# Optimization experiments

Hardware: AMD Instinct MI355X
Metric: run time of the kernel (lower is better)

## Reference

```python
import jax, jax.numpy as jnp
import numpy as np

N = 100000      # nodes
E = 1600000     # edges
NINP = 64       # input node features
NE = 8          # edge attr channels (spectral supports)
NOUT = 24       # nout1 == nout2
NIN = 2 * NOUT  # 48, hidden width after concat
G = 256         # graphs in batch
EPS = 1e-5


def setup_inputs() -> dict:
    key = jax.random.key(0)
    ks = jax.random.split(key, 40)
    def nrm(i, shape, s=1.0):
        return jax.random.normal(ks[i], shape, dtype=jnp.float32) * s
    inp = {}
    inp["x"] = nrm(0, (N, NINP))
    inp["edge_index"] = jax.random.randint(ks[1], (2, E), 0, N)
    inp["edge_attr"] = nrm(2, (E, NE))
    inp["batch"] = jnp.sort(jax.random.randint(ks[3], (N,), 0, G))
    i = 4
    for l, din in ((1, NINP), (2, NIN), (3, NIN)):
        inp[f"W{l}"] = nrm(i, (NE, din, NOUT), 0.1); i += 1   # SpectConv weight [K,in,out]
        inp[f"b{l}"] = jnp.zeros((NOUT,), jnp.float32)         # SpectConv bias
        inp[f"A{l}"] = nrm(i, (din, NOUT), 0.1); i += 1        # fc11 weight
        inp[f"a{l}"] = jnp.zeros((NOUT,), jnp.float32)
        inp[f"B{l}"] = nrm(i, (din, NOUT), 0.1); i += 1        # fc12 weight
        inp[f"c{l}"] = jnp.zeros((NOUT,), jnp.float32)
        inp[f"g{l}"] = jnp.ones((NIN,), jnp.float32)           # BN gamma
        inp[f"be{l}"] = jnp.zeros((NIN,), jnp.float32)         # BN beta
    inp["F1"] = nrm(i, (NIN, 32), 0.1); i += 1
    inp["f1"] = jnp.zeros((32,), jnp.float32)
    inp["F2"] = nrm(i, (32, 1), 0.1); i += 1
    inp["f2"] = jnp.zeros((1,), jnp.float32)
    return inp


def _ml3(x, src, dst, ea, W, b, A, a, Bm, c):
    # SpectConv (selfconn=False): sum_k segment_sum(ea[:,k]*x[src] -> dst) @ W[k] + b
    xs = x[src]                                    # [E, F] gather
    acc = jnp.zeros((x.shape[0], W.shape[2]), x.dtype)
    for k in range(W.shape[0]):                    # small fixed K=NE loop
        h = jax.ops.segment_sum(ea[:, k:k+1] * xs, dst, num_segments=x.shape[0])
        acc = acc + h @ W[k]
    conv = jax.nn.relu(acc + b)
    gate = jax.nn.relu(x @ A + a) * jnp.tanh(x @ Bm + c)
    return jnp.concatenate([conv, gate], axis=1)   # [N, NIN]


def _bn(x, g, b):
    # BatchNorm1d, training mode (biased batch statistics)
    m = x.mean(0)
    v = x.var(0)
    return (x - m) * jax.lax.rsqrt(v + EPS) * g + b


def reference(x, edge_index, edge_attr, batch,
              W1, b1, A1, a1, B1, c1, g1, be1,
              W2, b2, A2, a2, B2, c2, g2, be2,
              W3, b3, A3, a3, B3, c3, g3, be3,
              F1, f1, F2, f2):
    src, dst = edge_index[0], edge_index[1]
    h = _bn(_ml3(x, src, dst, edge_attr, W1, b1, A1, a1, B1, c1), g1, be1)
    h = _bn(_ml3(h, src, dst, edge_attr, W2, b2, A2, a2, B2, c2), g2, be2)
    h = _bn(_ml3(h, src, dst, edge_attr, W3, b3, A3, a3, B3, c3), g3, be3)
    sums = jax.ops.segment_sum(h, batch, num_segments=G)
    cnts = jax.ops.segment_sum(jnp.ones((h.shape[0], 1), h.dtype), batch, num_segments=G)
    pooled = sums / jnp.maximum(cnts, 1.0)         # global_mean_pool
    return jax.nn.relu(pooled @ F1 + f1) @ F2 + f2  # [G, 1]
```

## Files before the change

kernel.cpp:

```cpp
#include <hip/hip_runtime.h>
#include <hip/hip_fp16.h>
#include <math.h>

#define N_NODES 100000
#define N_EDGES 1600000
#define NGRAPH  256
#define YCOLS   240
#define EPS     1e-5f
#define BNCHUNK 200

typedef _Float16 h2v  __attribute__((ext_vector_type(2)));
typedef _Float16 f16x8 __attribute__((ext_vector_type(8)));
typedef float    f32x4 __attribute__((ext_vector_type(4)));

#if defined(__has_builtin)
#if __has_builtin(__builtin_amdgcn_fdot2)
#define HAVE_FDOT2 1
#endif
#endif

__device__ inline float dot8(float4 yraw, float4 eraw, float acc) {
#ifdef HAVE_FDOT2
  union U { float4 f; h2v v[4]; } y, e;
  y.f = yraw; e.f = eraw;
  acc = __builtin_amdgcn_fdot2(y.v[0], e.v[0], acc, false);
  acc = __builtin_amdgcn_fdot2(y.v[1], e.v[1], acc, false);
  acc = __builtin_amdgcn_fdot2(y.v[2], e.v[2], acc, false);
  acc = __builtin_amdgcn_fdot2(y.v[3], e.v[3], acc, false);
#else
  const __half2* yh = reinterpret_cast<const __half2*>(&yraw);
  const __half2* eh = reinterpret_cast<const __half2*>(&eraw);
#pragma unroll
  for (int i = 0; i < 4; i++) {
    float2 a = __half22float2(yh[i]), b = __half22float2(eh[i]);
    acc += a.x * b.x + a.y * b.y;
  }
#endif
  return acc;
}

__global__ void k_count(const int* __restrict__ dst, int* __restrict__ deg) {
  int e = blockIdx.x * blockDim.x + threadIdx.x;
  if (e < N_EDGES) atomicAdd(&deg[dst[e]], 1);
}

__global__ void k_scan1(const int* __restrict__ deg, int* __restrict__ part,
                        int* __restrict__ bsum) {
  __shared__ int lds[256];
  int t = threadIdx.x;
  int base = blockIdx.x * 1024 + t * 4;
  int v[4]; int s = 0;
#pragma unroll
  for (int i = 0; i < 4; i++) { int idx = base + i; v[i] = (idx < N_NODES) ? deg[idx] : 0; s += v[i]; }
  lds[t] = s; __syncthreads();
  for (int off = 1; off < 256; off <<= 1) {
    int x = (t >= off) ? lds[t - off] : 0;
    __syncthreads();
    lds[t] += x;
    __syncthreads();
  }
  int excl = lds[t] - s;
#pragma unroll
  for (int i = 0; i < 4; i++) { int idx = base + i; if (idx < N_NODES) part[idx] = excl; excl += v[i]; }
  if (t == 255) bsum[blockIdx.x] = lds[255];
}

__global__ void k_scan2(int* __restrict__ bsum, int nb) {
  __shared__ int lds[128];
  int t = threadIdx.x;
  int v = (t < nb) ? bsum[t] : 0;
  lds[t] = v; __syncthreads();
  for (int off = 1; off < 128; off <<= 1) {
    int x = (t >= off) ? lds[t - off] : 0;
    __syncthreads();
    lds[t] += x;
    __syncthreads();
  }
  if (t < nb) bsum[t] = lds[t] - v;
}

__global__ void k_scan3(int* __restrict__ rowptr, const int* __restrict__ bsum,
                        int* __restrict__ cursor) {
  int i = blockIdx.x * blockDim.x + threadIdx.x;
  if (i < N_NODES) {
    int v = rowptr[i] + bsum[i >> 10];
    rowptr[i] = v; cursor[i] = v;
  }
  if (i == 0) rowptr[N_NODES] = N_EDGES;
}

__global__ void k_fill(const int* __restrict__ src, const int* __restrict__ dst,
                       const float* __restrict__ ea, int* __restrict__ cursor,
                       int* __restrict__ esrc, __half* __restrict__ ea_csr) {
  int e = blockIdx.x * blockDim.x + threadIdx.x;
  if (e < N_EDGES) {
    int d = dst[e];
    int pos = atomicAdd(&cursor[d], 1);
    esrc[pos] = src[e];
    float4 a = *reinterpret_cast<const float4*>(ea + (size_t)e * 8);
    float4 b = *reinterpret_cast<const float4*>(ea + (size_t)e * 8 + 4);
    union { __half h[8]; float4 f; } u;
    u.h[0] = __float2half(a.x); u.h[1] = __float2half(a.y);
    u.h[2] = __float2half(a.z); u.h[3] = __float2half(a.w);
    u.h[4] = __float2half(b.x); u.h[5] = __float2half(b.y);
    u.h[6] = __float2half(b.z); u.h[7] = __float2half(b.w);
    *reinterpret_cast<float4*>(ea_csr + (size_t)pos * 8) = u.f;
  }
}

__global__ void k_ghist(const int* __restrict__ batch, int* __restrict__ gcnt) {
  __shared__ int lh[NGRAPH];
  int t = threadIdx.x;
  lh[t] = 0; __syncthreads();
  for (int i = blockIdx.x * 256 + t; i < N_NODES; i += gridDim.x * 256)
    atomicAdd(&lh[batch[i]], 1);
  __syncthreads();
  if (lh[t]) atomicAdd(&gcnt[t], lh[t]);
}

__global__ void k_gscan(const int* __restrict__ gcnt, int* __restrict__ gstart) {
  __shared__ int lds[NGRAPH];
  int t = threadIdx.x;
  int v = gcnt[t]; lds[t] = v; __syncthreads();
  for (int off = 1; off < NGRAPH; off <<= 1) {
    int x = (t >= off) ? lds[t - off] : 0;
    __syncthreads();
    lds[t] += x;
    __syncthreads();
  }
  gstart[t] = lds[t] - v;
  if (t == NGRAPH - 1) gstart[NGRAPH] = lds[NGRAPH - 1];
}

__global__ void k_wcat_h(const float* __restrict__ W, const float* __restrict__ A,
                         const float* __restrict__ B, __half* __restrict__ out,
                         int din) {
  int i = blockIdx.x * blockDim.x + threadIdx.x;
  if (i >= YCOLS * 64) return;
  int j = i / 64, f = i % 64;
  float v = 0.f;
  if (f < din) {
    if (j < 192)      { int k8 = j / 24, o = j - k8 * 24; v = W[(k8 * din + f) * 24 + o]; }
    else if (j < 216) v = A[f * 24 + (j - 192)];
    else              v = B[f * 24 + (j - 216)];
  }
  out[i] = __float2half(v);
}

template <int F>
__global__ __launch_bounds__(256) void k_mm(const float* __restrict__ X,
                                            const __half* __restrict__ Wct,
                                            const float* __restrict__ ss,
                                            const float* __restrict__ ba,
                                            const float* __restrict__ bc,
                                            __half* __restrict__ Yh,
                                            float* __restrict__ h) {
  __shared__ _Float16 sx[64][64];
  __shared__ _Float16 sy[64][200];
  __shared__ float    sg[64][52];
  int t = threadIdx.x;
  int r0 = blockIdx.x * 64;
  constexpr int F4 = F / 4;
  for (int i = t; i < 64 * F4; i += 256) {
    int row = i / F4, c4 = i - row * F4;
    int grow = r0 + row;
    float4 v = make_float4(0.f, 0.f, 0.f, 0.f);
    if (grow < N_NODES) {
      v = *reinterpret_cast<const float4*>(X + (size_t)grow * F + c4 * 4);
      if (ss) {
        int f = c4 * 4;
        v.x = v.x * ss[f + 0] + ss[48 + f + 0];
        v.y = v.y * ss[f + 1] + ss[48 + f + 1];
        v.z = v.z * ss[f + 2] + ss[48 + f + 2];
        v.w = v.w * ss[f + 3] + ss[48 + f + 3];
      }
    }
    int c = c4 * 4;
    sx[row][c + 0] = (_Float16)v.x;
    sx[row][c + 1] = (_Float16)v.y;
    sx[row][c + 2] = (_Float16)v.z;
    sx[row][c + 3] = (_Float16)v.w;
  }
  if (F == 48) {
    for (int i = t; i < 64 * 16; i += 256) {
      int row = i / 16, k = 48 + (i % 16);
      sx[row][k] = (_Float16)0.f;
    }
  }
  __syncthreads();

  int w = t >> 6, l = t & 63;
  int lrow = l & 15;
  int lk = (l >> 4) * 8;
  const f16x8 a0 = *reinterpret_cast<const f16x8*>(&sx[w * 16 + lrow][lk]);
  const f16x8 a1 = *reinterpret_cast<const f16x8*>(&sx[w * 16 + lrow][lk + 32]);
  const _Float16* wct = reinterpret_cast<const _Float16*>(Wct);

#pragma unroll
  for (int ct = 0; ct < 15; ct++) {
    int col = ct * 16 + lrow;
    f16x8 b0 = *reinterpret_cast<const f16x8*>(wct + col * 64 + lk);
    f16x8 b1 = *reinterpret_cast<const f16x8*>(wct + col * 64 + lk + 32);
    f32x4 acc = {0.f, 0.f, 0.f, 0.f};
    acc = __builtin_amdgcn_mfma_f32_16x16x32_f16(a0, b0, acc, 0, 0, 0);
    acc = __builtin_amdgcn_mfma_f32_16x16x32_f16(a1, b1, acc, 0, 0, 0);
    int ycol = (col % 24) * 8 + col / 24;
    int gc   = (col < 216) ? (col - 192) : (24 + col - 216);
#pragma unroll
    for (int r = 0; r < 4; r++) {
      int row = w * 16 + (l >> 4) * 4 + r;
      if (col < 192) sy[row][ycol] = (_Float16)acc[r];
      else           sg[row][gc] = acc[r];
    }
  }
  __syncthreads();

  int rows = N_NODES - r0; if (rows > 64) rows = 64;
  for (int i = t; i < rows * 48; i += 256) {
    int row = i / 48, c = (i % 48) * 4;
    *reinterpret_cast<uint2*>(Yh + (size_t)(r0 + row) * 192 + c) =
        *reinterpret_cast<const uint2*>(&sy[row][c]);
  }
  for (int i = t; i < rows * 24; i += 256) {
    int row = i / 24, o = i % 24;
    float gate = fmaxf(sg[row][o] + ba[o], 0.f) * tanhf(sg[row][24 + o] + bc[o]);
    h[(size_t)(r0 + row) * 48 + 24 + o] = gate;
  }
}

__global__ __launch_bounds__(192) void k_agg(
    const __half* __restrict__ Yh, const int* __restrict__ rowptr,
    const int* __restrict__ esrc, const __half* __restrict__ ea_csr,
    const float* __restrict__ bconv, float* __restrict__ h) {
  __shared__ float lacc[2][4][24];
  int t = threadIdx.x;
  int ln   = t / 96;
  int slot = (t / 24) % 4;
  int o    = t % 24;
  int n = blockIdx.x * 2 + ln;
  float acc = 0.f;
  if (n < N_NODES) {
    int r0 = rowptr[n], r1 = rowptr[n + 1];
    int idx = r0 + slot;
    for (; idx + 12 < r1; idx += 16) {
      int s0 = esrc[idx], s1 = esrc[idx + 4], s2 = esrc[idx + 8], s3 = esrc[idx + 12];
      float4 e0 = *reinterpret_cast<const float4*>(ea_csr + (size_t)idx * 8);
      float4 e1 = *reinterpret_cast<const float4*>(ea_csr + (size_t)(idx + 4) * 8);
      float4 e2 = *reinterpret_cast<const float4*>(ea_csr + (size_t)(idx + 8) * 8);
      float4 e3 = *reinterpret_cast<const float4*>(ea_csr + (size_t)(idx + 12) * 8);
      float4 y0 = *reinterpret_cast<const float4*>(Yh + (size_t)s0 * 192 + o * 8);
      float4 y1 = *reinterpret_cast<const float4*>(Yh + (size_t)s1 * 192 + o * 8);
      float4 y2 = *reinterpret_cast<const float4*>(Yh + (size_t)s2 * 192 + o * 8);
      float4 y3 = *reinterpret_cast<const float4*>(Yh + (size_t)s3 * 192 + o * 8);
      acc = dot8(y0, e0, acc);
      acc = dot8(y1, e1, acc);
      acc = dot8(y2, e2, acc);
      acc = dot8(y3, e3, acc);
    }
    for (; idx < r1; idx += 4) {
      int s0 = esrc[idx];
      float4 e0 = *reinterpret_cast<const float4*>(ea_csr + (size_t)idx * 8);
      float4 y0 = *reinterpret_cast<const float4*>(Yh + (size_t)s0 * 192 + o * 8);
      acc = dot8(y0, e0, acc);
    }
  }
  lacc[ln][slot][o] = acc;
  __syncthreads();
  if (t < 48) {
    int ln2 = t / 24, oo = t % 24;
    int n2 = blockIdx.x * 2 + ln2;
    if (n2 < N_NODES) {
      float a = lacc[ln2][0][oo] + lacc[ln2][1][oo] + lacc[ln2][2][oo] + lacc[ln2][3][oo];
      h[(size_t)n2 * 48 + oo] = fmaxf(a + bconv[oo], 0.f);
    }
  }
}

__global__ __launch_bounds__(192) void k_bnred1(const float* __restrict__ h,
                                                float* __restrict__ out) {
  __shared__ float lsum[192], lsq[192];
  int t = threadIdx.x;
  int rp = t / 48, c = t % 48;
  int r0 = blockIdx.x * BNCHUNK;
  int r1 = r0 + BNCHUNK; if (r1 > N_NODES) r1 = N_NODES;
  float s = 0.f, q = 0.f;
  for (int r = r0 + rp; r < r1; r += 4) {
    float v = h[(size_t)r * 48 + c];
    s += v; q += v * v;
  }
  lsum[t] = s; lsq[t] = q; __syncthreads();
  if (t < 48) {
    float S = lsum[t] + lsum[t + 48] + lsum[t + 96] + lsum[t + 144];
    float Q = lsq[t] + lsq[t + 48] + lsq[t + 96] + lsq[t + 144];
    out[(size_t)blockIdx.x * 96 + t] = S;
    out[(size_t)blockIdx.x * 96 + 48 + t] = Q;
  }
}

__global__ void k_bnstats(const float* __restrict__ partial, int nblk,
                          const float* __restrict__ g, const float* __restrict__ be,
                          float* __restrict__ ss) {
  __shared__ float ls[256], lq[256];
  int c = blockIdx.x, t = threadIdx.x;
  float s = 0.f, q = 0.f;
  for (int i = t; i < nblk; i += 256) { s += partial[(size_t)i * 96 + c]; q += partial[(size_t)i * 96 + 48 + c]; }
  ls[t] = s; lq[t] = q; __syncthreads();
  for (int off = 128; off > 0; off >>= 1) {
    if (t < off) { ls[t] += ls[t + off]; lq[t] += lq[t + off]; }
    __syncthreads();
  }
  if (t == 0) {
    float mean = ls[0] / (float)N_NODES;
    float var = lq[0] / (float)N_NODES - mean * mean;
    var = fmaxf(var, 0.f);
    float sc = g[c] * rsqrtf(var + EPS);
    ss[c] = sc;
    ss[48 + c] = be[c] - mean * sc;
  }
}

__global__ __launch_bounds__(240) void k_pool2(const float* __restrict__ h,
                                               const int* __restrict__ gstart,
                                               const float* __restrict__ ss,
                                               float* __restrict__ pooled) {
  __shared__ float acc[240];
  int g = blockIdx.x, t = threadIdx.x;
  int o = t % 48, r = t / 48;
  int n0 = gstart[g], n1 = gstart[g + 1];
  float s = 0.f;
  for (int n = n0 + r; n < n1; n += 5) s += h[(size_t)n * 48 + o];
  acc[t] = s; __syncthreads();
  if (t < 48) {
    float tot = acc[t] + acc[t + 48] + acc[t + 96] + acc[t + 144] + acc[t + 192];
    float cnt = (float)(n1 - n0);
    float mean = tot / fmaxf(cnt, 1.f);
    pooled[g * 48 + t] = mean * ss[t] + ss[48 + t];
  }
}

__global__ __launch_bounds__(64) void k_mlp(const float* __restrict__ pooled,
                                            const float* __restrict__ F1,
                                            const float* __restrict__ f1,
                                            const float* __restrict__ F2,
                                            const float* __restrict__ f2,
                                            float* __restrict__ out) {
  __shared__ float p[48];
  int g = blockIdx.x, t = threadIdx.x;
  if (t < 48) p[t] = pooled[g * 48 + t];
  __syncthreads();
  float r = 0.f;
  if (t < 32) {
    float s = f1[t];
#pragma unroll
    for (int c = 0; c < 48; c++) s += p[c] * F1[c * 32 + t];
    r = fmaxf(s, 0.f) * F2[t];
  }
  for (int off = 32; off > 0; off >>= 1) r += __shfl_down(r, off, 64);
  if (t == 0) out[g] = r + f2[0];
}

extern "C" void kernel_launch(void* const* d_in, const int* in_sizes, int n_in,
                              void* d_out, int out_size, void* d_ws, size_t ws_size,
                              hipStream_t stream) {
  const float* x          = (const float*)d_in[0];
  const int*   edge_index = (const int*)d_in[1];
  const float* ea         = (const float*)d_in[2];
  const int*   batch      = (const int*)d_in[3];
  const float *W[3], *bcv[3], *A[3], *ba[3], *B[3], *bc[3], *g[3], *be[3];
  for (int l = 0; l < 3; l++) {
    int base = 4 + l * 8;
    W[l]   = (const float*)d_in[base + 0];
    bcv[l] = (const float*)d_in[base + 1];
    A[l]   = (const float*)d_in[base + 2];
    ba[l]  = (const float*)d_in[base + 3];
    B[l]   = (const float*)d_in[base + 4];
    bc[l]  = (const float*)d_in[base + 5];
    g[l]   = (const float*)d_in[base + 6];
    be[l]  = (const float*)d_in[base + 7];
  }
  const float* F1 = (const float*)d_in[28];
  const float* f1 = (const float*)d_in[29];
  const float* F2 = (const float*)d_in[30];
  const float* f2 = (const float*)d_in[31];
  const int* src = edge_index;
  const int* dst = edge_index + N_EDGES;

  char* w = (char*)d_ws;
  auto alloc = [&](size_t bytes) -> char* {
    char* p = w;
    w += (bytes + 255) & ~(size_t)255;
    return p;
  };
  int nagg = (N_NODES + 1) / 2;
  int nred = (N_NODES + BNCHUNK - 1) / BNCHUNK;

  int*    rowptr  = (int*)alloc((N_NODES + 1) * 4);
  int*    cursor  = (int*)alloc((size_t)N_NODES * 4);
  int*    deg     = (int*)alloc((size_t)N_NODES * 4);
  int*    bsum    = (int*)alloc(128 * 4);
  int*    esrc    = (int*)alloc((size_t)N_EDGES * 4);
  __half* ea_csr  = (__half*)alloc((size_t)N_EDGES * 8 * 2);
  int*    gcnt    = (int*)alloc(NGRAPH * 4);
  int*    gstart  = (int*)alloc((NGRAPH + 1) * 4);
  __half* Wct1    = (__half*)alloc((size_t)YCOLS * 64 * 2);
  __half* Wct2    = (__half*)alloc((size_t)YCOLS * 64 * 2);
  __half* Wct3    = (__half*)alloc((size_t)YCOLS * 64 * 2);
  __half* Yh      = (__half*)alloc((size_t)N_NODES * 192 * 2);
  float*  h0      = (float*)alloc((size_t)N_NODES * 48 * 4);
  float*  h1      = (float*)alloc((size_t)N_NODES * 48 * 4);
  float*  partial2= (float*)alloc((size_t)nred * 96 * 4);
  float*  ss1     = (float*)alloc(96 * 4);
  float*  ss2     = (float*)alloc(96 * 4);
  float*  ss3     = (float*)alloc(96 * 4);
  float*  pooled  = (float*)alloc(NGRAPH * 48 * 4);

  hipMemsetAsync(deg, 0, (size_t)N_NODES * 4, stream);
  hipMemsetAsync(gcnt, 0, NGRAPH * 4, stream);

  k_count<<<(N_EDGES + 255) / 256, 256, 0, stream>>>(dst, deg);
  int nchunk = (N_NODES + 1023) / 1024;
  k_scan1<<<nchunk, 256, 0, stream>>>(deg, rowptr, bsum);
  k_scan2<<<1, 128, 0, stream>>>(bsum, nchunk);
  k_scan3<<<(N_NODES + 255) / 256, 256, 0, stream>>>(rowptr, bsum, cursor);
  k_fill<<<(N_EDGES + 255) / 256, 256, 0, stream>>>(src, dst, ea, cursor, esrc, ea_csr);

  k_ghist<<<64, 256, 0, stream>>>(batch, gcnt);
  k_gscan<<<1, NGRAPH, 0, stream>>>(gcnt, gstart);

  k_wcat_h<<<(YCOLS * 64 + 255) / 256, 256, 0, stream>>>(W[0], A[0], B[0], Wct1, 64);
  k_wcat_h<<<(YCOLS * 64 + 255) / 256, 256, 0, stream>>>(W[1], A[1], B[1], Wct2, 48);
  k_wcat_h<<<(YCOLS * 64 + 255) / 256, 256, 0, stream>>>(W[2], A[2], B[2], Wct3, 48);

  int nmm = (N_NODES + 63) / 64;

  k_mm<64><<<nmm, 256, 0, stream>>>(x, Wct1, nullptr, ba[0], bc[0], Yh, h0);
  k_agg<<<nagg, 192, 0, stream>>>(Yh, rowptr, esrc, ea_csr, bcv[0], h0);
  k_bnred1<<<nred, 192, 0, stream>>>(h0, partial2);
  k_bnstats<<<48, 256, 0, stream>>>(partial2, nred, g[0], be[0], ss1);
  k_mm<48><<<nmm, 256, 0, stream>>>(h0, Wct2, ss1, ba[1], bc[1], Yh, h1);
  k_agg<<<nagg, 192, 0, stream>>>(Yh, rowptr, esrc, ea_csr, bcv[1], h1);
  k_bnred1<<<nred, 192, 0, stream>>>(h1, partial2);
  k_bnstats<<<48, 256, 0, stream>>>(partial2, nred, g[1], be[1], ss2);
  k_mm<48><<<nmm, 256, 0, stream>>>(h1, Wct3, ss2, ba[2], bc[2], Yh, h0);
  k_agg<<<nagg, 192, 0, stream>>>(Yh, rowptr, esrc, ea_csr, bcv[2], h0);
  k_bnred1<<<nred, 192, 0, stream>>>(h0, partial2);
  k_bnstats<<<48, 256, 0, stream>>>(partial2, nred, g[2], be[2], ss3);

  k_pool2<<<NGRAPH, 240, 0, stream>>>(h0, gstart, ss3, pooled);
  k_mlp<<<NGRAPH, 64, 0, stream>>>(pooled, F1, f1, F2, f2, (float*)d_out);
}
```

Measured before the change: 645.8 us.

## Swap MFMA operands and store results directly from registers, dropping LDS staging

```diff
diff --git a/kernel.cpp b/kernel.cpp
--- a/kernel.cpp
+++ b/kernel.cpp
@@ -137,12 +137,14 @@
                          int din) {
   int i = blockIdx.x * blockDim.x + threadIdx.x;
   if (i >= YCOLS * 64) return;
-  int j = i / 64, f = i % 64;
+  int p = i / 64, f = i % 64;
   float v = 0.f;
   if (f < din) {
-    if (j < 192)      { int k8 = j / 24, o = j - k8 * 24; v = W[(k8 * din + f) * 24 + o]; }
-    else if (j < 216) v = A[f * 24 + (j - 192)];
-    else              v = B[f * 24 + (j - 216)];
+    if (p < 192) { int o = p >> 3, k8 = p & 7; v = W[(k8 * din + f) * 24 + o]; }
+    else {
+      int q = p - 192, o = q >> 1;
+      v = (q & 1) ? B[f * 24 + o] : A[f * 24 + o];
+    }
   }
   out[i] = __float2half(v);
 }
@@ -156,8 +158,6 @@
                                             __half* __restrict__ Yh,
                                             float* __restrict__ h) {
   __shared__ _Float16 sx[64][64];
-  __shared__ _Float16 sy[64][200];
-  __shared__ float    sg[64][52];
   int t = threadIdx.x;
   int r0 = blockIdx.x * 64;
   constexpr int F4 = F / 4;
@@ -190,41 +190,36 @@
   __syncthreads();
 
   int w = t >> 6, l = t & 63;
-  int lrow = l & 15;
+  int lo = l & 15;
   int lk = (l >> 4) * 8;
-  const f16x8 a0 = *reinterpret_cast<const f16x8*>(&sx[w * 16 + lrow][lk]);
-  const f16x8 a1 = *reinterpret_cast<const f16x8*>(&sx[w * 16 + lrow][lk + 32]);
+  int g  = l >> 4;
+  const f16x8 xb0 = *reinterpret_cast<const f16x8*>(&sx[w * 16 + lo][lk]);
+  const f16x8 xb1 = *reinterpret_cast<const f16x8*>(&sx[w * 16 + lo][lk + 32]);
   const _Float16* wct = reinterpret_cast<const _Float16*>(Wct);
+  int xg = r0 + w * 16 + lo;
 
 #pragma unroll
-  for (int ct = 0; ct < 15; ct++) {
-    int col = ct * 16 + lrow;
-    f16x8 b0 = *reinterpret_cast<const f16x8*>(wct + col * 64 + lk);
-    f16x8 b1 = *reinterpret_cast<const f16x8*>(wct + col * 64 + lk + 32);
+  for (int tt = 0; tt < 15; tt++) {
+    const f16x8 a0 = *reinterpret_cast<const f16x8*>(wct + (tt * 16 + lo) * 64 + lk);
+    const f16x8 a1 = *reinterpret_cast<const f16x8*>(wct + (tt * 16 + lo) * 64 + lk + 32);
     f32x4 acc = {0.f, 0.f, 0.f, 0.f};
-    acc = __builtin_amdgcn_mfma_f32_16x16x32_f16(a0, b0, acc, 0, 0, 0);
-    acc = __builtin_amdgcn_mfma_f32_16x16x32_f16(a1, b1, acc, 0, 0, 0);
-    int ycol = (col % 24) * 8 + col / 24;
-    int gc   = (col < 216) ? (col - 192) : (24 + col - 216);
-#pragma unroll
-    for (int r = 0; r < 4; r++) {
-      int row = w * 16 + (l >> 4) * 4 + r;
-      if (col < 192) sy[row][ycol] = (_Float16)acc[r];
-      else           sg[row][gc] = acc[r];
-    }
-  }
-  __syncthreads();
-
-  int rows = N_NODES - r0; if (rows > 64) rows = 64;
-  for (int i = t; i < rows * 48; i += 256) {
-    int row = i / 48, c = (i % 48) * 4;
-    *reinterpret_cast<uint2*>(Yh + (size_t)(r0 + row) * 192 + c) =
-        *reinterpret_cast<const uint2*>(&sy[row][c]);
-  }
-  for (int i = t; i < rows * 24; i += 256) {
-    int row = i / 24, o = i % 24;
-    float gate = fmaxf(sg[row][o] + ba[o], 0.f) * tanhf(sg[row][24 + o] + bc[o]);
-    h[(size_t)(r0 + row) * 48 + 24 + o] = gate;
+    acc = __builtin_amdgcn_mfma_f32_16x16x32_f16(a0, xb0, acc, 0, 0, 0);
+    acc = __builtin_amdgcn_mfma_f32_16x16x32_f16(a1, xb1, acc, 0, 0, 0);
+    if (xg < N_NODES) {
+      if (tt < 12) {
+        union { __half h4[4]; uint2 u; } pk;
+        pk.h4[0] = __float2half(acc[0]);
+        pk.h4[1] = __float2half(acc[1]);
+        pk.h4[2] = __float2half(acc[2]);
+        pk.h4[3] = __float2half(acc[3]);
+        *reinterpret_cast<uint2*>(Yh + (size_t)xg * 192 + tt * 16 + g * 4) = pk.u;
+      } else {
+        int o0 = (tt - 12) * 8 + g * 2;
+        float g0 = fmaxf(acc[0] + ba[o0], 0.f) * tanhf(acc[1] + bc[o0]);
+        float g1 = fmaxf(acc[2] + ba[o0 + 1], 0.f) * tanhf(acc[3] + bc[o0 + 1]);
+        *reinterpret_cast<float2*>(h + (size_t)xg * 48 + 24 + o0) = make_float2(g0, g1);
+      }
+    }
   }
 }
 
```

After: 637.5 us (median of 2 runs). Within noise of the previous version (-1.3%).
